# Kernel optimization log

Hardware: AMD Instinct MI355X
Metric: run time of the kernel (lower is better)

Reference implementation:

```python
import jax, jax.numpy as jnp
import numpy as np
from jax import lax

R, K = 1000, 80                 # proposals per image, foreground classes
IMG_H, IMG_W = 800.0, 1333.0    # image_shape (h, w) used by Boxes.clip
SCORE_THRESH = 0.05
NMS_THRESH = 0.5
TOPK = 100                      # topk_per_image


def setup_inputs() -> dict:
    key = jax.random.key(0)
    k1, k2, k3 = jax.random.split(key, 3)
    # well-formed class-specific boxes: x1y1 + positive wh
    x1y1 = jax.random.uniform(k1, (R, K, 2)) * jnp.array([IMG_W - 60.0, IMG_H - 60.0])
    wh = jax.random.uniform(k2, (R, K, 2)) * 200.0 + 10.0
    boxes = jnp.concatenate([x1y1, x1y1 + wh], axis=-1).reshape(R, K * 4)
    logits = jax.random.normal(k3, (R, K + 1)) * 2.0
    scores = jax.nn.softmax(logits, axis=-1)  # (R, K+1), last col = background
    return {"boxes": boxes, "scores": scores}


def _iou_matrix(b):
    # b: [R, 4] (x1, y1, x2, y2) -> [R, R] pairwise IoU
    x1, y1, x2, y2 = b[:, 0], b[:, 1], b[:, 2], b[:, 3]
    area = jnp.clip(x2 - x1, 0.0) * jnp.clip(y2 - y1, 0.0)
    xx1 = jnp.maximum(x1[:, None], x1[None, :])
    yy1 = jnp.maximum(y1[:, None], y1[None, :])
    xx2 = jnp.minimum(x2[:, None], x2[None, :])
    yy2 = jnp.minimum(y2[:, None], y2[None, :])
    inter = jnp.clip(xx2 - xx1, 0.0) * jnp.clip(yy2 - yy1, 0.0)
    union = area[:, None] + area[None, :] - inter
    return inter / jnp.maximum(union, 1e-9)


def _nms_one_class(boxes_c, scores_c, valid_c):
    # boxes_c: [R,4], scores_c: [R], valid_c: [R] bool (passed score filter)
    masked = jnp.where(valid_c, scores_c, -jnp.inf)
    order = jnp.argsort(-masked)            # descending score
    b = boxes_c[order]
    s = masked[order]
    v = valid_c[order]
    iou = iou_full = _iou_matrix(b)          # [R, R]
    idx = jnp.arange(R)

    def body(i, keep):
        # box i (if still kept & valid) suppresses later boxes with high IoU
        sup = (iou_full[i] > NMS_THRESH) & keep[i] & (idx > i)
        return keep & ~sup

    keep = lax.fori_loop(0, R, body, v)
    return s, keep, order


def reference(boxes, scores):
    # boxes: (R, K*4), scores: (R, K+1)
    bx = boxes.reshape(R, K, 4)
    # Boxes.clip(image_shape=(h, w)): x in [0, w], y in [0, h]
    bx = jnp.stack([
        jnp.clip(bx[..., 0], 0.0, IMG_W),
        jnp.clip(bx[..., 1], 0.0, IMG_H),
        jnp.clip(bx[..., 2], 0.0, IMG_W),
        jnp.clip(bx[..., 3], 0.0, IMG_H),
    ], axis=-1)

    fg = scores[:, :-1]                                  # (R, K) foreground scores
    thres = jnp.minimum(SCORE_THRESH, (fg.mean() + fg.max()) / 2.0)
    valid = fg > thres                                   # filter_mask

    # per-class batched NMS (equivalent to torchvision batched_nms)
    boxes_k = jnp.transpose(bx, (1, 0, 2))               # [K, R, 4]
    s_sorted, keep, order = jax.vmap(_nms_one_class)(boxes_k, fg.T, valid.T)

    flat = jnp.where(keep, s_sorted, -jnp.inf).reshape(-1)   # [K*R]
    topv, topi = lax.top_k(flat, TOPK)                   # keep[:topk], score-sorted
    cls = topi // R
    pos = topi % R
    prop = order[cls, pos]                               # original proposal index (filter_inds[:,0])
    ok = jnp.isfinite(topv)
    okf = ok.astype(boxes.dtype)

    box_out = bx[prop, cls] * okf[:, None]               # pred_boxes  [TOPK, 4]
    sc_out = jnp.where(ok, topv, 0.0)                    # scores      [TOPK]
    full_out = scores[prop] * okf[:, None]               # full_scores [TOPK, K+1]
    cls_out = (cls * ok).astype(boxes.dtype)             # pred_classes as float col

    # packed result: [boxes(4) | score(1) | class(1) | full_scores(K+1)]
    return jnp.concatenate([box_out, sc_out[:, None], cls_out[:, None], full_out], axis=1)
```

## Files before the change

kernel.cpp:

```cpp
#include <hip/hip_runtime.h>
#include <stdint.h>

typedef unsigned long long u64;
typedef unsigned int u32;

#define R_N 1000
#define K_N 80
#define NCOL 81
#define TOPK_N 100
#define OUT_W 87
#define IMG_W_ 1333.0f
#define IMG_H_ 800.0f
#define CSTR 100
#define CSTRP 101
#define NQUAD ((R_N * NCOL) / 4)
#define NMAX 448
#define WMAX 7
#define KM (K_N * CSTR)
#define POISON 0xAAAAAAAAu

__device__ __forceinline__ u32 f32_order(float f) {
    u32 u = __float_as_uint(f);
    return u ^ (((u32)((int)u >> 31)) | 0x80000000u);
}
__device__ __forceinline__ float f32_unorder(u32 o) {
    u32 u = (o & 0x80000000u) ? (o ^ 0x80000000u) : ~o;
    return __uint_as_float(u);
}

__device__ __forceinline__ void grid_barrier(u32* bar, u32 nblk) {
    __syncthreads();
    if (threadIdx.x == 0) {
        __threadfence();
        if (__hip_atomic_load(bar, __ATOMIC_RELAXED, __HIP_MEMORY_SCOPE_AGENT) == POISON)
            atomicCAS(bar, POISON, 0u);
        __hip_atomic_fetch_add(bar, 1u, __ATOMIC_ACQ_REL, __HIP_MEMORY_SCOPE_AGENT);
        while (__hip_atomic_load(bar, __ATOMIC_ACQUIRE, __HIP_MEMORY_SCOPE_AGENT) < nblk)
            __builtin_amdgcn_s_sleep(2);
    }
    __syncthreads();
}

struct P2 {
    float4 bx4[R_N];
    u64 key_s[R_N];
    u64 pool[NMAX * WMAX];
    float area[R_N];
    u64 keep_words[16];
    int s_n;
};
struct P3 {
    u64 keys[K_N * CSTRP];
    int rnk[TOPK_N];
    u64 wx[TOPK_N];
    int wr[TOPK_N];
    int wn;
};
union SMEM { P2 p2; P3 p3; };

__device__ void run_nms(int c, int tid, int lane, int wv, u64 below, float th,
                        const float* __restrict__ scores, P2& p2,
                        const float* __restrict__ boxes, u64* __restrict__ cand,
                        u32* __restrict__ kbs) {
    u64* ukey = p2.pool;
    if (wv == 0) {
        float sval[16];
#pragma unroll
        for (int e = 0; e < 16; ++e) {
            int r = e * 64 + lane;
            sval[e] = (r < R_N) ? scores[r * NCOL + c] : -1e30f;
        }
        int nn = 0;
#pragma unroll
        for (int e = 0; e < 16; ++e) {
            bool pred = sval[e] > th;
            u64 m = __ballot(pred);
            if (pred) {
                int r = e * 64 + lane;
                ukey[nn + __popcll(m & below)] =
                    ((u64)f32_order(sval[e]) << 32) | (u64)(u32)(R_N - 1 - r);
            }
            nn += __popcll(m);
        }
        if (lane == 0) p2.s_n = nn;
    }
    __syncthreads();
    const int n = p2.s_n;

    for (int j = tid; j < n; j += 256) {
        u64 kj = ukey[j];
        int rank = 0;
        for (int k = 0; k < n; ++k) rank += (ukey[k] > kj) ? 1 : 0;
        int r = (R_N - 1) - (int)(kj & 0xFFFFFFFFull);
        float4 b = ((const float4*)boxes)[r * K_N + c];
        float x1 = fminf(fmaxf(b.x, 0.f), IMG_W_);
        float y1 = fminf(fmaxf(b.y, 0.f), IMG_H_);
        float x2 = fminf(fmaxf(b.z, 0.f), IMG_W_);
        float y2 = fminf(fmaxf(b.w, 0.f), IMG_H_);
        p2.key_s[rank] = kj;
        p2.bx4[rank] = make_float4(x1, y1, x2, y2);
        p2.area[rank] = fmaxf(x2 - x1, 0.f) * fmaxf(y2 - y1, 0.f);
    }
    __syncthreads();

    if (n <= NMAX) {
        const int W = (n + 63) >> 6;
        u64* Mrow = p2.pool;
        const int nh = n >> 1;
        for (int t2 = wv; t2 < 2 * W; t2 += 4) {
            int w = t2 >> 1, ih = t2 & 1;
            int i0 = ih ? nh : 0;
            int i1 = ih ? n : nh;
            int j = w * 64 + lane;
            bool jv = j < n;
            float4 bj = jv ? p2.bx4[j] : make_float4(0.f, 0.f, 0.f, 0.f);
            float aj = jv ? p2.area[j] : 0.f;
            for (int i = i0; i < i1; ++i) {
                float4 bi = p2.bx4[i];
                float ai = p2.area[i];
                float xx1 = fmaxf(bi.x, bj.x), yy1 = fmaxf(bi.y, bj.y);
                float xx2 = fminf(bi.z, bj.z), yy2 = fminf(bi.w, bj.w);
                float inter = fmaxf(xx2 - xx1, 0.f) * fmaxf(yy2 - yy1, 0.f);
                bool sup = jv && (j > i) &&
                           (inter / fmaxf(ai + aj - inter, 1e-9f) > 0.5f);
                u64 m = __ballot(sup);
                if (lane == 0) Mrow[i * W + w] = m;
            }
        }
        __syncthreads();

        if (wv == 0) {
            u64 keep_w = 0;
            if (lane < W) {
                int rem = n - lane * 64;
                keep_w = (rem >= 64) ? ~0ull : ((1ull << rem) - 1ull);
            }
            const int lw = (lane < W) ? lane : 0;
            u64 fifo[8];
#pragma unroll
            for (int d = 0; d < 8; ++d) fifo[d] = (d < n) ? Mrow[d * W + lw] : 0ull;
            for (int ib = 0; ib < n; ib += 8) {
#pragma unroll
                for (int d = 0; d < 8; ++d) {
                    int i = ib + d;
                    if (i >= n) break;
                    u64 row = fifo[d];
                    int ip = i + 8;
                    fifo[d] = (ip < n) ? Mrow[ip * W + lw] : 0ull;
                    u64 kw = __shfl(keep_w, i >> 6);
                    if ((kw >> (i & 63)) & 1ull) keep_w &= ~row;
                }
            }
            if (lane < W) p2.keep_words[lane] = keep_w;
            if (lane >= W && lane < 16) p2.keep_words[lane] = 0;
        }
    } else {
        int* keep = (int*)p2.pool;
        for (int j = tid; j < n; j += 256) keep[j] = 1;
        __syncthreads();
        for (int i = 0; i < n - 1; ++i) {
            __syncthreads();
            if (!keep[i]) continue;
            float4 bi = p2.bx4[i];
            float ai = p2.area[i];
            for (int j = i + 1 + tid; j < n; j += 256) {
                if (!keep[j]) continue;
                float xx1 = fmaxf(bi.x, p2.bx4[j].x), yy1 = fmaxf(bi.y, p2.bx4[j].y);
                float xx2 = fminf(bi.z, p2.bx4[j].z), yy2 = fminf(bi.w, p2.bx4[j].w);
                float inter = fmaxf(xx2 - xx1, 0.f) * fmaxf(yy2 - yy1, 0.f);
                if (inter / fmaxf(ai + p2.area[j] - inter, 1e-9f) > 0.5f) keep[j] = 0;
            }
        }
        __syncthreads();
        if (wv == 0) {
            for (int w = 0; w < 16; ++w) {
                int j = w * 64 + lane;
                u64 m = __ballot((j < n) && keep[j]);
                if (lane == 0) p2.keep_words[w] = m;
            }
        }
    }
    __syncthreads();

    if (wv == 0) {
        int kb = 0;
        for (int j0 = 0; j0 < n; j0 += 64) {
            int j = j0 + lane;
            u64 mw = p2.keep_words[j0 >> 6];
            bool kp = (j < n) && ((mw >> lane) & 1ull);
            u64 mm = __ballot(kp);
            int kr = kb + __popcll(mm & below);
            if (kp && kr < CSTR) {
                u64 kj = p2.key_s[j];
                u32 osc = (u32)(kj >> 32);
                int rr = (R_N - 1) - (int)(kj & 0xFFFFFFFFull);
                int flat = c * R_N + j;
                cand[c * CSTR + kr] =
                    ((u64)osc << 27) | ((u64)(u32)(131071 - flat) << 10) | (u64)(u32)rr;
            }
            kb += __popcll(mm);
        }
        if (kb > CSTR) kb = CSTR;
        if (lane == 0) kbs[c] = (u32)kb;
        for (int kz = kb + lane; kz < CSTR; kz += 64) cand[c * CSTR + kz] = 0;
    }
}

__global__ __launch_bounds__(256, 1) void k_nms(const float* __restrict__ boxes,
                                                const float* __restrict__ scores,
                                                float* __restrict__ hdr,
                                                u32* __restrict__ kbs,
                                                u64* __restrict__ cand) {
    __shared__ P2 p2;
    __shared__ float s_sum[4], s_max[4];

    const int bid = blockIdx.x, tid = threadIdx.x;
    const int lane = tid & 63, wv = tid >> 6;
    const int c = bid;
    const u64 below = (lane == 0) ? 0ull : (~0ull >> (64 - lane));

    {
        float sum = 0.f, mx = -1e30f;
        int q = bid * 256 + tid;
        if (q < NQUAD) {
            float4 v = ((const float4*)scores)[q];
            int m = (q * 4) % NCOL;
            float vv[4] = {v.x, v.y, v.z, v.w};
#pragma unroll
            for (int e = 0; e < 4; ++e) {
                int mm = m + e; if (mm >= NCOL) mm -= NCOL;
                if (mm != K_N) { sum += vv[e]; mx = fmaxf(mx, vv[e]); }
            }
        }
#pragma unroll
        for (int off = 32; off > 0; off >>= 1) {
            sum += __shfl_down(sum, off);
            mx = fmaxf(mx, __shfl_down(mx, off));
        }
        if (lane == 0) { s_sum[wv] = sum; s_max[wv] = mx; }
        __syncthreads();
        if (tid == 0) {
            hdr[2 * bid] = s_sum[0] + s_sum[1] + s_sum[2] + s_sum[3];
            hdr[2 * bid + 1] = fmaxf(fmaxf(s_max[0], s_max[1]), fmaxf(s_max[2], s_max[3]));
        }
    }

    run_nms(c, tid, lane, wv, below, 0.05f, scores, p2, boxes, cand, kbs);
}

__global__ __launch_bounds__(256, 1) void k_top(const float* __restrict__ boxes,
                                                const float* __restrict__ scores,
                                                float* __restrict__ hdr,
                                                u32* __restrict__ kbs,
                                                u32* __restrict__ bars,
                                                u64* __restrict__ cand,
                                                float* __restrict__ outp) {
    __shared__ SMEM sm;
    __shared__ int s_cnt[2];
    __shared__ float s_thres;

    const int bid = blockIdx.x, tid = threadIdx.x;
    const int lane = tid & 63, wv = tid >> 6;
    const int c = bid;
    const u64 below = (lane == 0) ? 0ull : (~0ull >> (64 - lane));

    {
        const ulonglong2* cp = (const ulonglong2*)cand;
        for (int t = tid; t < KM / 2; t += 256) {
            ulonglong2 v = cp[t];
            int e0 = 2 * t;
            int cc2 = e0 / CSTR, pos = e0 - cc2 * CSTR;
            sm.p3.keys[cc2 * CSTRP + pos] = v.x;
            sm.p3.keys[cc2 * CSTRP + pos + 1] = v.y;
        }
    }
    u32 kcnt = (tid < K_N) ? kbs[tid] : 0u;
    {
        int cnt = (int)kcnt;
#pragma unroll
        for (int off = 32; off > 0; off >>= 1) cnt += __shfl_down(cnt, off);
        if (lane == 0 && wv < 2) s_cnt[wv] = cnt;
    }
    if (wv == 0) {
        float S = hdr[2 * lane], M = hdr[2 * lane + 1];
        if (lane + 64 < K_N) {
            S += hdr[2 * (lane + 64)];
            M = fmaxf(M, hdr[2 * (lane + 64) + 1]);
        }
#pragma unroll
        for (int off = 32; off > 0; off >>= 1) {
            S += __shfl_down(S, off);
            M = fmaxf(M, __shfl_down(M, off));
        }
        if (lane == 0)
            s_thres = fminf(0.05f, 0.5f * (S / (float)(R_N * K_N) + M));
    }
    __syncthreads();
    int total = s_cnt[0] + s_cnt[1];

    if (s_thres != 0.05f) {
        const float th = s_thres;
        run_nms(c, tid, lane, wv, below, th, scores, sm.p2, boxes, cand, kbs);
        grid_barrier(&bars[0], K_N);
        {
            const ulonglong2* cp = (const ulonglong2*)cand;
            for (int t = tid; t < KM / 2; t += 256) {
                ulonglong2 v = cp[t];
                int e0 = 2 * t;
                int cc2 = e0 / CSTR, pos = e0 - cc2 * CSTR;
                sm.p3.keys[cc2 * CSTRP + pos] = v.x;
                sm.p3.keys[cc2 * CSTRP + pos + 1] = v.y;
            }
            int cnt = (tid < K_N) ? (int)kbs[tid] : 0;
#pragma unroll
            for (int off = 32; off > 0; off >>= 1) cnt += __shfl_down(cnt, off);
            if (lane == 0 && wv < 2) s_cnt[wv] = cnt;
        }
        __syncthreads();
        total = s_cnt[0] + s_cnt[1];
    }

    const int target = total < TOPK_N ? total : TOPK_N;
    const int kb = (int)kbs[c];

    if (tid < TOPK_N) sm.p3.rnk[tid] = tid;
    if (tid == 0) sm.p3.wn = 0;
    __syncthreads();

    const int TASKS = kb * (K_N - 1);
    for (int g = 0; g * 2048 < TASKS; ++g) {
        int lo[8], hi[8], ii[8], base[8];
        u64 xv[8];
        bool act[8];
#pragma unroll
        for (int s = 0; s < 8; ++s) {
            int t = g * 2048 + s * 256 + tid;
            act[s] = t < TASKS;
            int i = 0, cc2 = 0;
            if (act[s]) { i = t % kb; cc2 = t / kb; }
            cc2 += (cc2 >= c);
            ii[s] = i;
            base[s] = cc2 * CSTRP;
            xv[s] = sm.p3.keys[c * CSTRP + i];
            if (xv[s] == 0ull) act[s] = false;
            lo[s] = 0; hi[s] = CSTR;
        }
#pragma unroll
        for (int st = 0; st < 7; ++st) {
#pragma unroll
            for (int s = 0; s < 8; ++s) {
                int mid = (lo[s] + hi[s]) >> 1;
                u64 v = sm.p3.keys[base[s] + mid];
                bool live = lo[s] < hi[s];
                bool gt = live && (v > xv[s]);
                lo[s] = gt ? mid + 1 : lo[s];
                hi[s] = (live && !gt) ? mid : hi[s];
            }
        }
#pragma unroll
        for (int s = 0; s < 8; ++s)
            if (act[s] && lo[s] > 0) atomicAdd(&sm.p3.rnk[ii[s]], lo[s]);
    }
    __syncthreads();

    if (tid < kb) {
        int r = sm.p3.rnk[tid];
        if (r < target) {
            int idx = atomicAdd(&sm.p3.wn, 1);
            sm.p3.wx[idx] = sm.p3.keys[c * CSTRP + tid];
            sm.p3.wr[idx] = r;
        }
    }
    __syncthreads();
    const int wn = sm.p3.wn;

    for (int e = tid; e < wn * OUT_W; e += 256) {
        int w = e / OUT_W, col = e - w * OUT_W;
        u64 x = sm.p3.wx[w];
        int r = sm.p3.wr[w];
        int prop = (int)(x & 0x3FFull);
        float val;
        if (col < 4) {
            float b = boxes[prop * (K_N * 4) + c * 4 + col];
            float lim = (col & 1) ? IMG_H_ : IMG_W_;
            val = fminf(fmaxf(b, 0.f), lim);
        } else if (col == 4) {
            val = f32_unorder((u32)((x >> 27) & 0xFFFFFFFFull));
        } else if (col == 5) {
            val = (float)c;
        } else {
            val = scores[prop * NCOL + (col - 6)];
        }
        outp[r * OUT_W + col] = val;
    }
    for (int row = target + bid; row < TOPK_N; row += K_N) {
        int ob = row * OUT_W;
        for (int e = tid; e < OUT_W; e += 256) outp[ob + e] = 0.f;
    }
}

extern "C" void kernel_launch(void* const* d_in, const int* in_sizes, int n_in,
                              void* d_out, int out_size, void* d_ws, size_t ws_size,
                              hipStream_t stream) {
    const float* boxes = (const float*)d_in[0];
    const float* scores = (const float*)d_in[1];
    float* hdr = (float*)d_ws;
    u32* kbs = (u32*)((char*)d_ws + 640);
    u32* bars = (u32*)((char*)d_ws + 960);
    u64* cand = (u64*)((char*)d_ws + 1024);

    k_nms<<<dim3(K_N), dim3(256), 0, stream>>>(boxes, scores, hdr, kbs, cand);
    k_top<<<dim3(K_N), dim3(256), 0, stream>>>(boxes, scores, hdr, kbs, bars, cand, (float*)d_out);
}
```

Before: 94.55 us.

## Inline NMS in k_nms with upfront score/box prefetch and shared-memory box staging

The hot-path NMS is inlined into k_nms. All global loads (class score column, class boxes, the stats quad) are issued at kernel start so their latencies overlap, and the boxes are staged into shared memory for the gather after sorting. The separate barrier between the stats reduction and key compaction is merged into one. k_top now reads its own class count from shared memory instead of a second global load. This adds register pressure and duplicates the NMS code, and the cold path keeps the old function.

```diff
diff --git a/kernel.cpp b/kernel.cpp
--- a/kernel.cpp
+++ b/kernel.cpp
@@ -58,10 +58,10 @@
 };
 union SMEM { P2 p2; P3 p3; };
 
-__device__ void run_nms(int c, int tid, int lane, int wv, u64 below, float th,
-                        const float* __restrict__ scores, P2& p2,
-                        const float* __restrict__ boxes, u64* __restrict__ cand,
-                        u32* __restrict__ kbs) {
+__device__ void run_nms_cold(int c, int tid, int lane, int wv, u64 below, float th,
+                             const float* __restrict__ scores, P2& p2,
+                             const float* __restrict__ boxes, u64* __restrict__ cand,
+                             u32* __restrict__ kbs) {
     u64* ukey = p2.pool;
     if (wv == 0) {
         float sval[16];
@@ -219,13 +219,30 @@
     const int c = bid;
     const u64 below = (lane == 0) ? 0ull : (~0ull >> (64 - lane));
 
+    float sval[16];
+    if (wv == 0) {
+#pragma unroll
+        for (int e = 0; e < 16; ++e) {
+            int r = e * 64 + lane;
+            sval[e] = (r < R_N) ? scores[r * NCOL + c] : -1e30f;
+        }
+    }
+    float4 breg[4];
+#pragma unroll
+    for (int e = 0; e < 4; ++e) {
+        int r = tid + e * 256;
+        breg[e] = (r < R_N) ? ((const float4*)boxes)[r * K_N + c]
+                            : make_float4(0.f, 0.f, 0.f, 0.f);
+    }
+    const int q = bid * 256 + tid;
+    float4 qv = (q < NQUAD) ? ((const float4*)scores)[q]
+                            : make_float4(0.f, 0.f, 0.f, 0.f);
+
     {
         float sum = 0.f, mx = -1e30f;
-        int q = bid * 256 + tid;
         if (q < NQUAD) {
-            float4 v = ((const float4*)scores)[q];
             int m = (q * 4) % NCOL;
-            float vv[4] = {v.x, v.y, v.z, v.w};
+            float vv[4] = {qv.x, qv.y, qv.z, qv.w};
 #pragma unroll
             for (int e = 0; e < 4; ++e) {
                 int mm = m + e; if (mm >= NCOL) mm -= NCOL;
@@ -238,14 +255,152 @@
             mx = fmaxf(mx, __shfl_down(mx, off));
         }
         if (lane == 0) { s_sum[wv] = sum; s_max[wv] = mx; }
-        __syncthreads();
-        if (tid == 0) {
-            hdr[2 * bid] = s_sum[0] + s_sum[1] + s_sum[2] + s_sum[3];
-            hdr[2 * bid + 1] = fmaxf(fmaxf(s_max[0], s_max[1]), fmaxf(s_max[2], s_max[3]));
-        }
-    }
-
-    run_nms(c, tid, lane, wv, below, 0.05f, scores, p2, boxes, cand, kbs);
+    }
+
+    float4* bstage = (float4*)p2.pool;
+#pragma unroll
+    for (int e = 0; e < 4; ++e) {
+        int r = tid + e * 256;
+        if (r < R_N) bstage[r] = breg[e];
+    }
+    u64* ukey = p2.pool + 2000;
+    if (wv == 0) {
+        int nn = 0;
+#pragma unroll
+        for (int e = 0; e < 16; ++e) {
+            bool pred = sval[e] > 0.05f;
+            u64 m = __ballot(pred);
+            if (pred) {
+                int r = e * 64 + lane;
+                ukey[nn + __popcll(m & below)] =
+                    ((u64)f32_order(sval[e]) << 32) | (u64)(u32)(R_N - 1 - r);
+            }
+            nn += __popcll(m);
+        }
+        if (lane == 0) p2.s_n = nn;
+    }
+    __syncthreads();
+    if (tid == 0) {
+        hdr[2 * bid] = s_sum[0] + s_sum[1] + s_sum[2] + s_sum[3];
+        hdr[2 * bid + 1] = fmaxf(fmaxf(s_max[0], s_max[1]), fmaxf(s_max[2], s_max[3]));
+    }
+    const int n = p2.s_n;
+
+    for (int j = tid; j < n; j += 256) {
+        u64 kj = ukey[j];
+        int rank = 0;
+        for (int k = 0; k < n; ++k) rank += (ukey[k] > kj) ? 1 : 0;
+        int r = (R_N - 1) - (int)(kj & 0xFFFFFFFFull);
+        float4 b = bstage[r];
+        float x1 = fminf(fmaxf(b.x, 0.f), IMG_W_);
+        float y1 = fminf(fmaxf(b.y, 0.f), IMG_H_);
+        float x2 = fminf(fmaxf(b.z, 0.f), IMG_W_);
+        float y2 = fminf(fmaxf(b.w, 0.f), IMG_H_);
+        p2.key_s[rank] = kj;
+        p2.bx4[rank] = make_float4(x1, y1, x2, y2);
+        p2.area[rank] = fmaxf(x2 - x1, 0.f) * fmaxf(y2 - y1, 0.f);
+    }
+    __syncthreads();
+
+    if (n <= NMAX) {
+        const int W = (n + 63) >> 6;
+        u64* Mrow = p2.pool;
+        for (int t2 = wv; t2 < 4 * W; t2 += 4) {
+            int w = t2 >> 2, qh = t2 & 3;
+            int i0 = (n * qh) >> 2;
+            int i1 = (n * (qh + 1)) >> 2;
+            int j = w * 64 + lane;
+            bool jv = j < n;
+            float4 bj = jv ? p2.bx4[j] : make_float4(0.f, 0.f, 0.f, 0.f);
+            float aj = jv ? p2.area[j] : 0.f;
+            for (int i = i0; i < i1; ++i) {
+                float4 bi = p2.bx4[i];
+                float ai = p2.area[i];
+                float xx1 = fmaxf(bi.x, bj.x), yy1 = fmaxf(bi.y, bj.y);
+                float xx2 = fminf(bi.z, bj.z), yy2 = fminf(bi.w, bj.w);
+                float inter = fmaxf(xx2 - xx1, 0.f) * fmaxf(yy2 - yy1, 0.f);
+                bool sup = jv && (j > i) &&
+                           (inter / fmaxf(ai + aj - inter, 1e-9f) > 0.5f);
+                u64 m = __ballot(sup);
+                if (lane == 0) Mrow[i * W + w] = m;
+            }
+        }
+        __syncthreads();
+
+        if (wv == 0) {
+            u64 keep_w = 0;
+            if (lane < W) {
+                int rem = n - lane * 64;
+                keep_w = (rem >= 64) ? ~0ull : ((1ull << rem) - 1ull);
+            }
+            const int lw = (lane < W) ? lane : 0;
+            u64 fifo[8];
+#pragma unroll
+            for (int d = 0; d < 8; ++d) fifo[d] = (d < n) ? Mrow[d * W + lw] : 0ull;
+            for (int ib = 0; ib < n; ib += 8) {
+#pragma unroll
+                for (int d = 0; d < 8; ++d) {
+                    int i = ib + d;
+                    if (i >= n) break;
+                    u64 row = fifo[d];
+                    int ip = i + 8;
+                    fifo[d] = (ip < n) ? Mrow[ip * W + lw] : 0ull;
+                    u64 kw = __shfl(keep_w, i >> 6);
+                    if ((kw >> (i & 63)) & 1ull) keep_w &= ~row;
+                }
+            }
+            if (lane < W) p2.keep_words[lane] = keep_w;
+            if (lane >= W && lane < 16) p2.keep_words[lane] = 0;
+        }
+    } else {
+        int* keep = (int*)p2.pool;
+        for (int j = tid; j < n; j += 256) keep[j] = 1;
+        __syncthreads();
+        for (int i = 0; i < n - 1; ++i) {
+            __syncthreads();
+            if (!keep[i]) continue;
+            float4 bi = p2.bx4[i];
+            float ai = p2.area[i];
+            for (int j = i + 1 + tid; j < n; j += 256) {
+                if (!keep[j]) continue;
+                float xx1 = fmaxf(bi.x, p2.bx4[j].x), yy1 = fmaxf(bi.y, p2.bx4[j].y);
+                float xx2 = fminf(bi.z, p2.bx4[j].z), yy2 = fminf(bi.w, p2.bx4[j].w);
+                float inter = fmaxf(xx2 - xx1, 0.f) * fmaxf(yy2 - yy1, 0.f);
+                if (inter / fmaxf(ai + p2.area[j] - inter, 1e-9f) > 0.5f) keep[j] = 0;
+            }
+        }
+        __syncthreads();
+        if (wv == 0) {
+            for (int w = 0; w < 16; ++w) {
+                int j = w * 64 + lane;
+                u64 m = __ballot((j < n) && keep[j]);
+                if (lane == 0) p2.keep_words[w] = m;
+            }
+        }
+    }
+
+    if (wv == 0) {
+        int kb = 0;
+        for (int j0 = 0; j0 < n; j0 += 64) {
+            int j = j0 + lane;
+            u64 mw = p2.keep_words[j0 >> 6];
+            bool kp = (j < n) && ((mw >> lane) & 1ull);
+            u64 mm = __ballot(kp);
+            int kr = kb + __popcll(mm & below);
+            if (kp && kr < CSTR) {
+                u64 kj = p2.key_s[j];
+                u32 osc = (u32)(kj >> 32);
+                int rr = (R_N - 1) - (int)(kj & 0xFFFFFFFFull);
+                int flat = c * R_N + j;
+                cand[c * CSTR + kr] =
+                    ((u64)osc << 27) | ((u64)(u32)(131071 - flat) << 10) | (u64)(u32)rr;
+            }
+            kb += __popcll(mm);
+        }
+        if (kb > CSTR) kb = CSTR;
+        if (lane == 0) kbs[c] = (u32)kb;
+        for (int kz = kb + lane; kz < CSTR; kz += 64) cand[c * CSTR + kz] = 0;
+    }
 }
 
 __global__ __launch_bounds__(256, 1) void k_top(const float* __restrict__ boxes,
@@ -257,6 +412,7 @@
                                                 float* __restrict__ outp) {
     __shared__ SMEM sm;
     __shared__ int s_cnt[2];
+    __shared__ int s_kbc;
     __shared__ float s_thres;
 
     const int bid = blockIdx.x, tid = threadIdx.x;
@@ -275,6 +431,7 @@
         }
     }
     u32 kcnt = (tid < K_N) ? kbs[tid] : 0u;
+    if (tid == c) s_kbc = (int)kcnt;
     {
         int cnt = (int)kcnt;
 #pragma unroll
@@ -300,7 +457,7 @@
 
     if (s_thres != 0.05f) {
         const float th = s_thres;
-        run_nms(c, tid, lane, wv, below, th, scores, sm.p2, boxes, cand, kbs);
+        run_nms_cold(c, tid, lane, wv, below, th, scores, sm.p2, boxes, cand, kbs);
         grid_barrier(&bars[0], K_N);
         {
             const ulonglong2* cp = (const ulonglong2*)cand;
@@ -312,6 +469,7 @@
                 sm.p3.keys[cc2 * CSTRP + pos + 1] = v.y;
             }
             int cnt = (tid < K_N) ? (int)kbs[tid] : 0;
+            if (tid == c) s_kbc = cnt;
 #pragma unroll
             for (int off = 32; off > 0; off >>= 1) cnt += __shfl_down(cnt, off);
             if (lane == 0 && wv < 2) s_cnt[wv] = cnt;
@@ -321,7 +479,7 @@
     }
 
     const int target = total < TOPK_N ? total : TOPK_N;
-    const int kb = (int)kbs[c];
+    const int kb = s_kbc;
 
     if (tid < TOPK_N) sm.p3.rnk[tid] = tid;
     if (tid == 0) sm.p3.wn = 0;
```

Result: no change. 93.98 us (-0.6%).
